# Kernel optimization log

Measured on AMD Instinct MI355X. Metric: run time of the kernel, lower is better.

The kernel has to match this reference:

```python
import jax, jax.numpy as jnp
import numpy as np

GH = 16           # graph_hidden_features
D_IN = 2 * GH     # 32, concat(embed, lin)
D_H = 32          # hidden_features1
D_OUT = 16        # output_features1
NU, NC, E, L = 500000, 10000, 2000000, 500000


def _sage(x_src, x_dst, e_src, e_dst, Wl, bl, Wr, n_dst):
    # PyG SAGEConv: lin_l(mean_{j in N(i)} x_j) + lin_r(x_i); lin_r has no bias
    msg = x_src[e_src]                                   # [E, d]
    agg = jax.ops.segment_sum(msg, e_dst, num_segments=n_dst)
    cnt = jax.ops.segment_sum(jnp.ones((e_dst.shape[0],), msg.dtype), e_dst, num_segments=n_dst)
    agg = agg / jnp.maximum(cnt, 1.0)[:, None]
    return agg @ Wl.T + bl + x_dst @ Wr.T


def setup_inputs() -> dict:
    key = jax.random.key(0)
    ks = jax.random.split(key, 32)
    s = 0.05
    inp = {
        'user_x': jax.random.normal(ks[0], (NU, 5), jnp.float32),
        'course_x': jax.random.normal(ks[1], (NC, 2), jnp.float32),
        'user_embed': jax.random.normal(ks[2], (NU, GH), jnp.float32) * s,
        'course_embed': jax.random.normal(ks[3], (NC, GH), jnp.float32) * s,
        'Wu': jax.random.normal(ks[4], (GH, 5), jnp.float32) * s,
        'bu': jnp.zeros((GH,), jnp.float32),
        'Wc': jax.random.normal(ks[5], (GH, 2), jnp.float32) * s,
        'bc': jnp.zeros((GH,), jnp.float32),
        # conv1, edge type ('user','enroll','course')
        'c1e_Wl': jax.random.normal(ks[6], (D_H, D_IN), jnp.float32) * s,
        'c1e_bl': jnp.zeros((D_H,), jnp.float32),
        'c1e_Wr': jax.random.normal(ks[7], (D_H, D_IN), jnp.float32) * s,
        # conv1, edge type ('course','rev_enroll','user')
        'c1r_Wl': jax.random.normal(ks[8], (D_H, D_IN), jnp.float32) * s,
        'c1r_bl': jnp.zeros((D_H,), jnp.float32),
        'c1r_Wr': jax.random.normal(ks[9], (D_H, D_IN), jnp.float32) * s,
        # conv2 per edge type
        'c2e_Wl': jax.random.normal(ks[10], (D_OUT, D_H), jnp.float32) * s,
        'c2e_bl': jnp.zeros((D_OUT,), jnp.float32),
        'c2e_Wr': jax.random.normal(ks[11], (D_OUT, D_H), jnp.float32) * s,
        'c2r_Wl': jax.random.normal(ks[12], (D_OUT, D_H), jnp.float32) * s,
        'c2r_bl': jnp.zeros((D_OUT,), jnp.float32),
        'c2r_Wr': jax.random.normal(ks[13], (D_OUT, D_H), jnp.float32) * s,
        'user_node_index': jnp.arange(NU, dtype=jnp.int64) if jax.config.jax_enable_x64 else jnp.arange(NU, dtype=jnp.int32),
        'course_node_index': jnp.arange(NC, dtype=jnp.int32),
        'edge_src': jax.random.randint(ks[14], (E,), 0, NU, jnp.int32),
        'edge_dst': jax.random.randint(ks[15], (E,), 0, NC, jnp.int32),
        'label_src': jax.random.randint(ks[16], (L,), 0, NU, jnp.int32),
        'label_dst': jax.random.randint(ks[17], (L,), 0, NC, jnp.int32),
    }
    return inp


def reference(user_x, course_x, user_embed, course_embed, Wu, bu, Wc, bc,
              c1e_Wl, c1e_bl, c1e_Wr, c1r_Wl, c1r_bl, c1r_Wr,
              c2e_Wl, c2e_bl, c2e_Wr, c2r_Wl, c2r_bl, c2r_Wr,
              user_node_index, course_node_index, edge_src, edge_dst,
              label_src, label_dst):
    n_u, n_c = user_x.shape[0], course_x.shape[0]
    # feature fusion: concat(embedding lookup, linear projection)  -> [N, 32]
    xu = jnp.concatenate([user_embed[user_node_index], user_x @ Wu.T + bu], axis=1)
    xc = jnp.concatenate([course_embed[course_node_index], course_x @ Wc.T + bc], axis=1)
    # layer 1 (to_hetero: separate SAGEConv params per edge type, one edge type per dst)
    hc = jax.nn.relu(_sage(xu, xc, edge_src, edge_dst, c1e_Wl, c1e_bl, c1e_Wr, n_c))
    hu = jax.nn.relu(_sage(xc, xu, edge_dst, edge_src, c1r_Wl, c1r_bl, c1r_Wr, n_u))
    # layer 2
    oc = _sage(hu, hc, edge_src, edge_dst, c2e_Wl, c2e_bl, c2e_Wr, n_c)
    ou = _sage(hc, hu, edge_dst, edge_src, c2r_Wl, c2r_bl, c2r_Wr, n_u)
    # dot-product decode on labeled edges
    return (ou[label_src] * oc[label_dst]).sum(axis=-1)
```

## Files before the change

kernel.cpp:

```cpp
#include <hip/hip_runtime.h>

#define THREADS 256
#define CSH 6
#define USH 12
#define MAXBIN 192

typedef _Float16 half8 __attribute__((ext_vector_type(8)));
typedef _Float16 half4 __attribute__((ext_vector_type(4)));
typedef float floatx4 __attribute__((ext_vector_type(4)));

static __device__ __forceinline__ int imax(int a, int b){ return a > b ? a : b; }
static __device__ __forceinline__ int imin(int a, int b){ return a < b ? a : b; }


__global__ __launch_bounds__(256) void k_phase0(const int* __restrict__ es, const int* __restrict__ ed,
                                                int* __restrict__ cnt_c, int* __restrict__ cnt_u,
                                                int E, int NBC, int NBU){
    __shared__ int hc[MAXBIN], hu[MAXBIN];
    int t = threadIdx.x;
    int base = blockIdx.x * 2048 + t;
    if (t < MAXBIN){ hc[t] = 0; hu[t] = 0; }
    __syncthreads();
    #pragma unroll
    for (int k = 0; k < 8; k++){
        int i = base + k * 256;
        if (i < E){
            int s = __builtin_nontemporal_load(&es[i]);
            int d = __builtin_nontemporal_load(&ed[i]);
            atomicAdd(&hc[d >> CSH], 1); atomicAdd(&hu[s >> USH], 1);
        }
    }
    __syncthreads();
    if (t < NBC && hc[t]) atomicAdd(&cnt_c[t], hc[t]);
    if (t < NBU && hu[t]) atomicAdd(&cnt_u[t], hu[t]);
}

__global__ void k_sbase(const int* __restrict__ cnt_c, const int* __restrict__ cnt_u,
                        int* __restrict__ base_c, int* __restrict__ cur_c,
                        int* __restrict__ base_u, int* __restrict__ cur_u,
                        int* __restrict__ off_c, int* __restrict__ off_u,
                        int NC, int NU, int NBC, int NBU, int E){
    if (threadIdx.x == 0){
        int a = 0;
        for (int b = 0; b < NBC; b++){ base_c[b] = a; cur_c[b] = a; a += cnt_c[b]; }
        a = 0;
        for (int b = 0; b < NBU; b++){ base_u[b] = a; cur_u[b] = a; a += cnt_u[b]; }
        off_c[NC] = E; off_u[NU] = E;
    }
}

__global__ __launch_bounds__(256) void k_phase1(const int* __restrict__ es, const int* __restrict__ ed,
                                                int* __restrict__ cur_c, int* __restrict__ cur_u,
                                                uint2* __restrict__ binned_c, uint2* __restrict__ binned_u,
                                                int E, int NBC, int NBU){
    __shared__ uint2 stc[2048], stu[2048];
    __shared__ int hc[MAXBIN], scc[MAXBIN], lcc[MAXBIN], gbc[MAXBIN];
    __shared__ int hu[MAXBIN], scu[MAXBIN], lcu[MAXBIN], gbu[MAXBIN];
    int t = threadIdx.x;
    int base = blockIdx.x * 2048 + t;
    int s[8], d[8];
    #pragma unroll
    for (int k = 0; k < 8; k++){
        int i = base + k * 256;
        if (i < E){ s[k] = __builtin_nontemporal_load(&es[i]); d[k] = __builtin_nontemporal_load(&ed[i]); }
    }
    if (t < MAXBIN){ hc[t] = 0; hu[t] = 0; }
    __syncthreads();
    #pragma unroll
    for (int k = 0; k < 8; k++){
        int i = base + k * 256;
        if (i < E){ atomicAdd(&hc[d[k] >> CSH], 1); atomicAdd(&hu[s[k] >> USH], 1); }
    }
    __syncthreads();
    if (t == 0){ int a = 0; for (int b = 0; b < NBC; b++){ scc[b] = a; a += hc[b]; } }
    if (t == 1){ int a = 0; for (int b = 0; b < NBU; b++){ scu[b] = a; a += hu[b]; } }
    __syncthreads();
    if (t < NBC){ lcc[t] = scc[t]; gbc[t] = atomicAdd(&cur_c[t], hc[t]); }
    if (t < NBU){ lcu[t] = scu[t]; gbu[t] = atomicAdd(&cur_u[t], hu[t]); }
    __syncthreads();
    #pragma unroll
    for (int k = 0; k < 8; k++){
        int i = base + k * 256;
        if (i < E){
            int p = atomicAdd(&lcc[d[k] >> CSH], 1); stc[p] = make_uint2((unsigned)s[k], (unsigned)d[k]);
            int q = atomicAdd(&lcu[s[k] >> USH], 1); stu[q] = make_uint2((unsigned)s[k], (unsigned)d[k]);
        }
    }
    __syncthreads();
    int nv = imin(2048, E - blockIdx.x * 2048);
    for (int i = t; i < nv; i += 256){
        uint2 e = stc[i]; int b  = (int)(e.y >> CSH); binned_c[gbc[b]  + (i - scc[b])]  = e;
        uint2 f = stu[i]; int b2 = (int)(f.x >> USH); binned_u[gbu[b2] + (i - scu[b2])] = f;
    }
}

__global__ __launch_bounds__(1024) void k_p2(const uint2* __restrict__ binned_c, const uint2* __restrict__ binned_u,
                                             const int* __restrict__ cnt_c, const int* __restrict__ base_c,
                                             const int* __restrict__ cnt_u, const int* __restrict__ base_u,
                                             int* __restrict__ off_c, int* __restrict__ csr_c,
                                             int* __restrict__ off_u, int* __restrict__ csr_u,
                                             int NC, int NU, int NBC){
    __shared__ int lsh[5120];
    int t = threadIdx.x;
    const int CB = 1 << CSH;
    if ((int)blockIdx.x < NBC){
        int b = blockIdx.x;
        int* lh  = lsh;
        int* lof = lsh + CB;
        if (t < CB) lh[t] = 0;
        __syncthreads();
        int n = cnt_c[b], gb = base_c[b];
        const uint2* src = binned_c + gb;
        for (int i = t; i < n; i += 1024) atomicAdd(&lh[src[i].y & (CB - 1)], 1);
        __syncthreads();
        if (t == 0){ int a = gb; for (int c = 0; c < CB; c++){ lof[c] = a; a += lh[c]; } }
        __syncthreads();
        int gc = (b << CSH) + t;
        if (t < CB && gc < NC) off_c[gc] = lof[t];
        __syncthreads();
        for (int i = t; i < n; i += 1024){
            uint2 e = src[i];
            int p = atomicAdd(&lof[e.y & (CB - 1)], 1);
            csr_c[p] = (int)e.x;
        }
    } else {
        int b = blockIdx.x - NBC;
        const int UB = 1 << USH;
        int* lh   = lsh;
        int* part = lsh + UB;
        for (int i = t; i < UB; i += 1024) lh[i] = 0;
        __syncthreads();
        int n = cnt_u[b], gb = base_u[b];
        const uint2* src = binned_u + gb;
        for (int i = t; i < n; i += 1024) atomicAdd(&lh[src[i].x & (UB - 1)], 1);
        __syncthreads();
        int ps = lh[t * 4] + lh[t * 4 + 1] + lh[t * 4 + 2] + lh[t * 4 + 3];
        part[t] = ps;
        __syncthreads();
        for (int dd = 1; dd < 1024; dd <<= 1){
            int v = (t >= dd) ? part[t - dd] : 0;
            __syncthreads();
            if (t >= dd) part[t] += v;
            __syncthreads();
        }
        int a2 = gb + (t ? part[t - 1] : 0);
        #pragma unroll
        for (int j = 0; j < 4; j++){ int idx = t * 4 + j; int tmp = lh[idx]; lh[idx] = a2; a2 += tmp; }
        __syncthreads();
        int ub = b << USH;
        for (int i = t; i < UB; i += 1024){ int gu = ub + i; if (gu < NU) off_u[gu] = lh[i]; }
        __syncthreads();
        for (int i = t; i < n; i += 1024){
            uint2 e = src[i];
            int p = atomicAdd(&lh[e.x & (UB - 1)], 1);
            csr_u[p] = (int)e.y;
        }
    }
}


__global__ __launch_bounds__(256) void k_xu16(const float* __restrict__ uemb, const int* __restrict__ uidx,
                                              const float* __restrict__ ux, _Float16* __restrict__ xu16, int NU){
    int u = blockIdx.x * blockDim.x + threadIdx.x;
    if (u >= NU) return;
    const float4* er = (const float4*)(uemb + (size_t)uidx[u] * 16);
    float4 e0 = er[0], e1 = er[1], e2 = er[2], e3 = er[3];
    _Float16 h[32];
    h[0]=(_Float16)e0.x; h[1]=(_Float16)e0.y; h[2]=(_Float16)e0.z; h[3]=(_Float16)e0.w;
    h[4]=(_Float16)e1.x; h[5]=(_Float16)e1.y; h[6]=(_Float16)e1.z; h[7]=(_Float16)e1.w;
    h[8]=(_Float16)e2.x; h[9]=(_Float16)e2.y; h[10]=(_Float16)e2.z; h[11]=(_Float16)e2.w;
    h[12]=(_Float16)e3.x; h[13]=(_Float16)e3.y; h[14]=(_Float16)e3.z; h[15]=(_Float16)e3.w;
    const float* xr = ux + (size_t)u * 5;
    h[16]=(_Float16)xr[0]; h[17]=(_Float16)xr[1]; h[18]=(_Float16)xr[2]; h[19]=(_Float16)xr[3]; h[20]=(_Float16)xr[4];
    #pragma unroll
    for (int q = 21; q < 32; q++) h[q] = (_Float16)0.f;
    float4* out = (float4*)(xu16 + (size_t)u * 32);
    const float4* hv = (const float4*)h;
    out[0] = hv[0]; out[1] = hv[1]; out[2] = hv[2]; out[3] = hv[3];
}


__global__ void k_wprep(const float* __restrict__ Wl, const float* __restrict__ bl,
                        const float* __restrict__ Wr, const float* __restrict__ Wu,
                        const float* __restrict__ bu,
                        const float* __restrict__ Acoef, const float* __restrict__ Bcoef,
                        _Float16* __restrict__ wB1a, _Float16* __restrict__ wB1b,
                        _Float16* __restrict__ wB2, float* __restrict__ whb){
    int t = threadIdx.x;
    if (t < 128){
        int nt = t >> 6, l = t & 63;
        int ur = l & 15, kg = l >> 4, o = nt * 16 + ur;
        _Float16* pa = wB1a + (size_t)(nt * 64 + l) * 8;
        _Float16* pb = wB1b + (size_t)(nt * 64 + l) * 8;
        #pragma unroll
        for (int j = 0; j < 8; j++){
            pa[j] = (_Float16)Wl[o * 32 + kg * 8 + j];
            int k = kg * 8 + j;
            float v;
            if (k < 16) v = Wr[o * 32 + k];
            else if (k < 21){
                int pc = k - 16; float s = 0.f;
                for (int m = 0; m < 16; m++) s += Wr[o * 32 + 16 + m] * Wu[m * 5 + pc];
                v = s;
            } else v = 0.f;
            pb[j] = (_Float16)v;
        }
        const float* W = nt ? Bcoef : Acoef;
        _Float16* p2 = wB2 + (size_t)(nt * 64 + l) * 8;
        #pragma unroll
        for (int j = 0; j < 8; j++) p2[j] = (_Float16)W[ur * 32 + kg * 8 + j];
    } else if (t < 160){
        int o = t - 128;
        float s = bl[o];
        for (int m = 0; m < 16; m++) s += Wr[o * 32 + 16 + m] * bu[m];
        whb[o] = s;
    }
}


__global__ void k_xc(const float* __restrict__ cx, const float* __restrict__ cemb,
                     const int* __restrict__ cidx, const float* __restrict__ Wc,
                     const float* __restrict__ bc, float* __restrict__ xc,
                     _Float16* __restrict__ xc16, int NC){
    int i = blockIdx.x * blockDim.x + threadIdx.x;
    if (i >= NC * 32) return;
    int c = i >> 5, f = i & 31;
    float v;
    if (f < 16) v = cemb[cidx[c] * 16 + f];
    else { int o = f - 16; v = bc[o] + cx[c * 2 + 0] * Wc[o * 2 + 0] + cx[c * 2 + 1] * Wc[o * 2 + 1]; }
    xc[i] = v;
    xc16[i] = (_Float16)v;
}


__global__ __launch_bounds__(256) void k_course_l1(
    const int* __restrict__ off_c, const int* __restrict__ csr_c,
    const _Float16* __restrict__ xu16,
    const float* __restrict__ Wu, const float* __restrict__ bu,
    const float* __restrict__ Wl, const float* __restrict__ bl, const float* __restrict__ Wr,
    const float* __restrict__ Acoef , const float* __restrict__ Bcoef ,
    const float* __restrict__ xc,
    _Float16* __restrict__ hc2r16, float* __restrict__ hcWr, int NC)
{
    __shared__ float sWlT[1024], sWrT[1024], sAT[512], sBT[512], sWu[80], sbu[16], sbl[32];
    __shared__ float part[256];
    __shared__ float agg[32], aggx[8], hc[32];
    int t = threadIdx.x;
    for (int i = t; i < 1024; i += 256){ int o = i >> 5, k = i & 31; sWlT[k * 32 + o] = Wl[i]; sWrT[k * 32 + o] = Wr[i]; }
    for (int i = t; i < 512;  i += 256){ int j = i >> 5, o = i & 31; sAT[o * 16 + j] = Acoef[i]; sBT[o * 16 + j] = Bcoef[i]; }
    if (t < 80) sWu[t] = Wu[t];
    if (t < 16) sbu[t] = bu[t];
    if (t < 32) sbl[t] = bl[t];
    __syncthreads();
    int el = t >> 5, f = t & 31;
    for (int c = blockIdx.x; c < NC; c += gridDim.x){
        int lo = off_c[c], hi = off_c[c + 1];
        float acc = 0.f;
        int j = lo + el;
        for (; j + 24 < hi; j += 32){
            int s0 = csr_c[j], s1 = csr_c[j + 8], s2 = csr_c[j + 16], s3 = csr_c[j + 24];
            acc += (float)xu16[(size_t)s0 * 32 + f] + (float)xu16[(size_t)s1 * 32 + f]
                 + (float)xu16[(size_t)s2 * 32 + f] + (float)xu16[(size_t)s3 * 32 + f];
        }
        for (; j < hi; j += 8) acc += (float)xu16[(size_t)csr_c[j] * 32 + f];
        part[t] = acc; __syncthreads();
        float inv = 1.f / (float)imax(hi - lo, 1);
        if (el == 0 && f < 21){
            float s2 = part[f];
            #pragma unroll
            for (int k = 1; k < 8; k++) s2 += part[k * 32 + f];
            s2 *= inv;
            if (f < 16) agg[f] = s2; else aggx[f - 16] = s2;
        }
        __syncthreads();
        if (t < 16){
            float d = sbu[t];
            #pragma unroll
            for (int k = 0; k < 5; k++) d += aggx[k] * sWu[t * 5 + k];
            agg[16 + t] = d;
        }
        __syncthreads();
        if (t < 32){
            float h = sbl[t];
            for (int k = 0; k < 32; k++) h += agg[k] * sWlT[k * 32 + t] + xc[c * 32 + k] * sWrT[k * 32 + t];
            hc[t] = fmaxf(h, 0.f);
        }
        __syncthreads();
        if (t < 16){
            float a = 0.f, b = 0.f;
            for (int o = 0; o < 32; o++){ float h = hc[o]; a += h * sAT[o * 16 + t]; b += h * sBT[o * 16 + t]; }
            hc2r16[c * 16 + t] = (_Float16)a; hcWr[c * 16 + t] = b;
        }
        __syncthreads();
    }
}


__global__ __launch_bounds__(256) void k_user_mfma(
    const int* __restrict__ off_u, const int* __restrict__ csr_u,
    const _Float16* __restrict__ xc16, const _Float16* __restrict__ hc2r16,
    const _Float16* __restrict__ xu16,
    const _Float16* __restrict__ wB1a, const _Float16* __restrict__ wB1b,
    const _Float16* __restrict__ wB2, const float* __restrict__ whb,
    const float* __restrict__ bl2 ,
    _Float16* __restrict__ hu2e, float* __restrict__ ou, int NU)
{
    const int t = threadIdx.x;
    const int w = t >> 6, l = t & 63;
    const int ur = l & 15;
    const int kg = l >> 4;

    half8 b1[2][2], b2[2];
    b1[0][0] = *(const half8*)(wB1a + (size_t)l * 8);
    b1[0][1] = *(const half8*)(wB1a + (size_t)(64 + l) * 8);
    b1[1][0] = *(const half8*)(wB1b + (size_t)l * 8);
    b1[1][1] = *(const half8*)(wB1b + (size_t)(64 + l) * 8);
    b2[0]    = *(const half8*)(wB2  + (size_t)l * 8);
    b2[1]    = *(const half8*)(wB2  + (size_t)(64 + l) * 8);
    float hbias[2] = { whb[ur], whb[16 + ur] };
    const float bl2v = bl2[ur];

    __shared__ float lds_all[4][16 * 36 + 16 * 20];
    float* hl  = lds_all[w];
    float* b0l = lds_all[w] + 16 * 36;

    const int stride = gridDim.x * 64;
    for (int u0 = blockIdx.x * 64 + w * 16; u0 < NU; u0 += stride){
        int u = u0 + ur;
        int lo = 0, n = 0;
        if (u < NU){ lo = off_u[u]; n = off_u[u + 1] - lo; }
        float a[8] = {0,0,0,0,0,0,0,0};
        float p4[4] = {0,0,0,0};
        int j = 0;
        while (__any(j < n)){
            int d0 = (j     < n) ? csr_u[lo + j]     : -1;
            int d1 = (j + 1 < n) ? csr_u[lo + j + 1] : -1;
            if (d0 >= 0){
                half8 xv = *(const half8*)(xc16 + (size_t)d0 * 32 + kg * 8);
                half4 hv = *(const half4*)(hc2r16 + (size_t)d0 * 16 + kg * 4);
                #pragma unroll
                for (int q = 0; q < 8; q++) a[q] += (float)xv[q];
                #pragma unroll
                for (int q = 0; q < 4; q++) p4[q] += (float)hv[q];
            }
            if (d1 >= 0){
                half8 xv = *(const half8*)(xc16 + (size_t)d1 * 32 + kg * 8);
                half4 hv = *(const half4*)(hc2r16 + (size_t)d1 * 16 + kg * 4);
                #pragma unroll
                for (int q = 0; q < 8; q++) a[q] += (float)xv[q];
                #pragma unroll
                for (int q = 0; q < 4; q++) p4[q] += (float)hv[q];
            }
            j += 2;
        }
        float inv = 1.f / (float)imax(n, 1);
        half8 a1, a2;
        #pragma unroll
        for (int q = 0; q < 8; q++) a1[q] = (_Float16)(a[q] * inv);
        #pragma unroll
        for (int q = 0; q < 8; q++) a2[q] = (_Float16)0.f;
        if (u < NU) a2 = *(const half8*)(xu16 + (size_t)u * 32 + kg * 8);
        floatx4 c1[2];
        #pragma unroll
        for (int nt = 0; nt < 2; nt++){
            floatx4 c = {hbias[nt], hbias[nt], hbias[nt], hbias[nt]};
            c = __builtin_amdgcn_mfma_f32_16x16x32_f16(a1, b1[0][nt], c, 0, 0, 0);
            c = __builtin_amdgcn_mfma_f32_16x16x32_f16(a2, b1[1][nt], c, 0, 0, 0);
            c1[nt] = c;
        }
        asm volatile("s_waitcnt lgkmcnt(0)" ::: "memory");
        #pragma unroll
        for (int nt = 0; nt < 2; nt++)
            #pragma unroll
            for (int r = 0; r < 4; r++)
                hl[(kg * 4 + r) * 36 + nt * 16 + ur] = fmaxf(c1[nt][r], 0.f);
        #pragma unroll
        for (int q = 0; q < 4; q++) b0l[ur * 20 + kg * 4 + q] = p4[q] * inv;
        asm volatile("s_waitcnt lgkmcnt(0)" ::: "memory");
        half8 ah;
        {
            const float* hp = hl + ur * 36 + kg * 8;
            #pragma unroll
            for (int q = 0; q < 8; q++) ah[q] = (_Float16)hp[q];
        }
        floatx4 c20 = {0.f, 0.f, 0.f, 0.f};
        c20 = __builtin_amdgcn_mfma_f32_16x16x32_f16(ah, b2[0], c20, 0, 0, 0);
        floatx4 c21 = {bl2v, bl2v, bl2v, bl2v};
        c21 = __builtin_amdgcn_mfma_f32_16x16x32_f16(ah, b2[1], c21, 0, 0, 0);
        #pragma unroll
        for (int r = 0; r < 4; r++){
            int urow = kg * 4 + r;
            int ug = u0 + urow;
            if (ug < NU){
                hu2e[(size_t)ug * 16 + ur] = (_Float16)c20[r];
                ou[(size_t)ug * 16 + ur]   = c21[r] + b0l[urow * 20 + ur];
            }
        }
    }
}


__global__ __launch_bounds__(256) void k_course_l2(
    const int* __restrict__ off_c, const int* __restrict__ csr_c,
    const _Float16* __restrict__ hu2e, const float* __restrict__ bl2,
    const float* __restrict__ hcWr, float* __restrict__ oc, int NC)
{
    __shared__ float part[256];
    int t = threadIdx.x; int el = t >> 4, f = t & 15;
    for (int c = blockIdx.x; c < NC; c += gridDim.x){
        int lo = off_c[c], hi = off_c[c + 1];
        float acc = 0.f;
        int j = lo + el;
        for (; j + 48 < hi; j += 64){
            acc += (float)hu2e[(size_t)csr_c[j] * 16 + f] + (float)hu2e[(size_t)csr_c[j + 16] * 16 + f]
                 + (float)hu2e[(size_t)csr_c[j + 32] * 16 + f] + (float)hu2e[(size_t)csr_c[j + 48] * 16 + f];
        }
        for (; j < hi; j += 16) acc += (float)hu2e[(size_t)csr_c[j] * 16 + f];
        part[t] = acc; __syncthreads();
        if (el == 0){
            float s = part[f];
            #pragma unroll
            for (int k = 1; k < 16; k++) s += part[k * 16 + f];
            oc[c * 16 + f] = s / (float)imax(hi - lo, 1) + bl2[f] + hcWr[c * 16 + f];
        }
        __syncthreads();
    }
}


__global__ void k_decode(const int* __restrict__ ls, const int* __restrict__ ld,
                         const float* __restrict__ ou, const float* __restrict__ oc,
                         float* __restrict__ out, int L){
    int gt = blockIdx.x * blockDim.x + threadIdx.x;
    int l = gt >> 2, q = gt & 3;
    if (l >= L) return;
    int a = ls[l], b = ld[l];
    float4 va = ((const float4*)(ou + (size_t)a * 16))[q];
    float4 vb = ((const float4*)(oc + (size_t)b * 16))[q];
    float s = va.x * vb.x + va.y * vb.y + va.z * vb.z + va.w * vb.w;
    s += __shfl_xor(s, 1);
    s += __shfl_xor(s, 2);
    if (q == 0) out[l] = s;
}


extern "C" void kernel_launch(void* const* d_in, const int* in_sizes, int n_in,
                              void* d_out, int out_size, void* d_ws, size_t ws_size,
                              hipStream_t stream)
{
    const float* user_x       = (const float*)d_in[0];
    const float* course_x     = (const float*)d_in[1];
    const float* user_embed   = (const float*)d_in[2];
    const float* course_embed = (const float*)d_in[3];
    const float* Wu = (const float*)d_in[4];
    const float* bu = (const float*)d_in[5];
    const float* Wc = (const float*)d_in[6];
    const float* bc = (const float*)d_in[7];
    const float* c1e_Wl = (const float*)d_in[8];
    const float* c1e_bl = (const float*)d_in[9];
    const float* c1e_Wr = (const float*)d_in[10];
    const float* c1r_Wl = (const float*)d_in[11];
    const float* c1r_bl = (const float*)d_in[12];
    const float* c1r_Wr = (const float*)d_in[13];
    const float* c2e_Wl = (const float*)d_in[14];
    const float* c2e_bl = (const float*)d_in[15];
    const float* c2e_Wr = (const float*)d_in[16];
    const float* c2r_Wl = (const float*)d_in[17];
    const float* c2r_bl = (const float*)d_in[18];
    const float* c2r_Wr = (const float*)d_in[19];
    const int* uidx      = (const int*)d_in[20];
    const int* cidx      = (const int*)d_in[21];
    const int* edge_src  = (const int*)d_in[22];
    const int* edge_dst  = (const int*)d_in[23];
    const int* label_src = (const int*)d_in[24];
    const int* label_dst = (const int*)d_in[25];
    const int NU = in_sizes[20], NC = in_sizes[21], E = in_sizes[22], L = in_sizes[24];
    const int NBC = (NC + (1 << CSH) - 1) >> CSH;
    const int NBU = (NU + (1 << USH) - 1) >> USH;

    char* ws = (char*)d_ws;
    size_t woff = 0;
    auto alloc = [&](size_t bytes) -> char* {
        char* p = ws + woff;
        woff = (woff + bytes + 255) & ~(size_t)255;
        return p;
    };
    int*   off_u = (int*)  alloc((size_t)(NU + 1) * 4);
    int*   off_c = (int*)  alloc((size_t)(NC + 1) * 4);
    int*   csr_c = (int*)  alloc((size_t)E * 4);
    int*   csr_u = (int*)  alloc((size_t)E * 4);
    float* xc    = (float*)alloc((size_t)NC * 32 * 4);
    _Float16* xc16 = (_Float16*)alloc((size_t)NC * 32 * 2);
    _Float16* hc2r16 = (_Float16*)alloc((size_t)NC * 16 * 2);
    float* hcWr  = (float*)alloc((size_t)NC * 16 * 4);
    _Float16* hu2e = (_Float16*)alloc((size_t)NU * 16 * 2);
    float* ou    = (float*)alloc((size_t)NU * 16 * 4);
    float* occ   = (float*)alloc((size_t)NC * 16 * 4);
    _Float16* xu16 = (_Float16*)alloc((size_t)NU * 32 * 2);
    _Float16* wB1a = (_Float16*)alloc(1024 * 2);
    _Float16* wB1b = (_Float16*)alloc(1024 * 2);
    _Float16* wB2  = (_Float16*)alloc(1024 * 2);
    float* whb     = (float*)alloc(32 * 4);
    int*   cnt_c  = (int*) alloc(MAXBIN * 4);
    int*   cnt_u  = (int*) alloc(MAXBIN * 4);
    int*   base_c = (int*) alloc(MAXBIN * 4);
    int*   base_u = (int*) alloc(MAXBIN * 4);
    int*   cur_c  = (int*) alloc(MAXBIN * 4);
    int*   cur_u  = (int*) alloc(MAXBIN * 4);
    uint2* binned_c = (uint2*)hu2e;
    uint2* binned_u = (uint2*)ou;
    (void)ws_size; (void)n_in; (void)out_size;

    int chunks = (E + 2047) / 2048;

    hipMemsetAsync(cnt_c, 0, MAXBIN * 4, stream);
    hipMemsetAsync(cnt_u, 0, MAXBIN * 4, stream);
    k_phase0<<<chunks, 256, 0, stream>>>(edge_src, edge_dst, cnt_c, cnt_u, E, NBC, NBU);
    k_wprep<<<1, 256, 0, stream>>>(c1r_Wl, c1r_bl, c1r_Wr, Wu, bu, c2e_Wl, c2r_Wr, wB1a, wB1b, wB2, whb);
    k_xu16<<<(NU + 255) / 256, 256, 0, stream>>>(user_embed, uidx, user_x, xu16, NU);
    k_sbase<<<1, 64, 0, stream>>>(cnt_c, cnt_u, base_c, cur_c, base_u, cur_u, off_c, off_u, NC, NU, NBC, NBU, E);
    k_phase1<<<chunks, 256, 0, stream>>>(edge_src, edge_dst, cur_c, cur_u, binned_c, binned_u, E, NBC, NBU);
    k_xc<<<(NC * 32 + 255) / 256, 256, 0, stream>>>(course_x, course_embed, cidx, Wc, bc, xc, xc16, NC);
    k_p2<<<NBC + NBU, 1024, 0, stream>>>(binned_c, binned_u, cnt_c, base_c, cnt_u, base_u,
                                         off_c, csr_c, off_u, csr_u, NC, NU, NBC);
    k_course_l1<<<2048, 256, 0, stream>>>(off_c, csr_c, xu16, Wu, bu,
                                          c1e_Wl, c1e_bl, c1e_Wr, c2r_Wl, c2e_Wr, xc, hc2r16, hcWr, NC);
    k_user_mfma<<<1024, 256, 0, stream>>>(off_u, csr_u, xc16, hc2r16, xu16,
                                          wB1a, wB1b, wB2, whb, c2r_bl, hu2e, ou, NU);
    k_course_l2<<<2048, 256, 0, stream>>>(off_c, csr_c, hu2e, c2e_bl, hcWr, occ, NC);
    k_decode<<<(unsigned)(((size_t)L * 4 + 255) / 256), 256, 0, stream>>>(label_src, label_dst, ou, occ, (float*)d_out, L);
}
```

Measured before the change: 307.9 us.

## Store user output in fp16, unroll gather by four, double user kernel grid

The user-side output ou is now stored as fp16 instead of fp32, which halves its write traffic in k_user_mfma and its read traffic in k_decode. The user neighbor-gather loop now processes four edges per iteration instead of two, giving more loads in flight. The user kernel grid is doubled to 2048 blocks. Because ou no longer aliases the binned_u scratch buffer, binned_u gets its own workspace allocation, which needs more workspace memory and adds fp16 rounding error to the final dot products.

```diff
diff --git a/kernel.cpp b/kernel.cpp
--- a/kernel.cpp
+++ b/kernel.cpp
@@ -303,7 +303,7 @@
     const _Float16* __restrict__ wB1a, const _Float16* __restrict__ wB1b,
     const _Float16* __restrict__ wB2, const float* __restrict__ whb,
     const float* __restrict__ bl2 ,
-    _Float16* __restrict__ hu2e, float* __restrict__ ou, int NU)
+    _Float16* __restrict__ hu2e, _Float16* __restrict__ ou, int NU)
 {
     const int t = threadIdx.x;
     const int w = t >> 6, l = t & 63;
@@ -335,6 +335,8 @@
         while (__any(j < n)){
             int d0 = (j     < n) ? csr_u[lo + j]     : -1;
             int d1 = (j + 1 < n) ? csr_u[lo + j + 1] : -1;
+            int d2 = (j + 2 < n) ? csr_u[lo + j + 2] : -1;
+            int d3 = (j + 3 < n) ? csr_u[lo + j + 3] : -1;
             if (d0 >= 0){
                 half8 xv = *(const half8*)(xc16 + (size_t)d0 * 32 + kg * 8);
                 half4 hv = *(const half4*)(hc2r16 + (size_t)d0 * 16 + kg * 4);
@@ -351,7 +353,23 @@
                 #pragma unroll
                 for (int q = 0; q < 4; q++) p4[q] += (float)hv[q];
             }
-            j += 2;
+            if (d2 >= 0){
+                half8 xv = *(const half8*)(xc16 + (size_t)d2 * 32 + kg * 8);
+                half4 hv = *(const half4*)(hc2r16 + (size_t)d2 * 16 + kg * 4);
+                #pragma unroll
+                for (int q = 0; q < 8; q++) a[q] += (float)xv[q];
+                #pragma unroll
+                for (int q = 0; q < 4; q++) p4[q] += (float)hv[q];
+            }
+            if (d3 >= 0){
+                half8 xv = *(const half8*)(xc16 + (size_t)d3 * 32 + kg * 8);
+                half4 hv = *(const half4*)(hc2r16 + (size_t)d3 * 16 + kg * 4);
+                #pragma unroll
+                for (int q = 0; q < 8; q++) a[q] += (float)xv[q];
+                #pragma unroll
+                for (int q = 0; q < 4; q++) p4[q] += (float)hv[q];
+            }
+            j += 4;
         }
         float inv = 1.f / (float)imax(n, 1);
         half8 a1, a2;
@@ -393,7 +411,7 @@
             int ug = u0 + urow;
             if (ug < NU){
                 hu2e[(size_t)ug * 16 + ur] = (_Float16)c20[r];
-                ou[(size_t)ug * 16 + ur]   = c21[r] + b0l[urow * 20 + ur];
+                ou[(size_t)ug * 16 + ur]   = (_Float16)(c21[r] + b0l[urow * 20 + ur]);
             }
         }
     }
@@ -429,15 +447,15 @@
 
 
 __global__ void k_decode(const int* __restrict__ ls, const int* __restrict__ ld,
-                         const float* __restrict__ ou, const float* __restrict__ oc,
+                         const _Float16* __restrict__ ou, const float* __restrict__ oc,
                          float* __restrict__ out, int L){
     int gt = blockIdx.x * blockDim.x + threadIdx.x;
     int l = gt >> 2, q = gt & 3;
     if (l >= L) return;
     int a = ls[l], b = ld[l];
-    float4 va = ((const float4*)(ou + (size_t)a * 16))[q];
+    half4 va = *(const half4*)(ou + (size_t)a * 16 + q * 4);
     float4 vb = ((const float4*)(oc + (size_t)b * 16))[q];
-    float s = va.x * vb.x + va.y * vb.y + va.z * vb.z + va.w * vb.w;
+    float s = (float)va[0] * vb.x + (float)va[1] * vb.y + (float)va[2] * vb.z + (float)va[3] * vb.w;
     s += __shfl_xor(s, 1);
     s += __shfl_xor(s, 2);
     if (q == 0) out[l] = s;
@@ -494,7 +512,8 @@
     _Float16* hc2r16 = (_Float16*)alloc((size_t)NC * 16 * 2);
     float* hcWr  = (float*)alloc((size_t)NC * 16 * 4);
     _Float16* hu2e = (_Float16*)alloc((size_t)NU * 16 * 2);
-    float* ou    = (float*)alloc((size_t)NU * 16 * 4);
+    _Float16* ou   = (_Float16*)alloc((size_t)NU * 16 * 2);
+    uint2* binned_u = (uint2*)alloc((size_t)E * 8);
     float* occ   = (float*)alloc((size_t)NC * 16 * 4);
     _Float16* xu16 = (_Float16*)alloc((size_t)NU * 32 * 2);
     _Float16* wB1a = (_Float16*)alloc(1024 * 2);
@@ -508,7 +527,6 @@
     int*   cur_c  = (int*) alloc(MAXBIN * 4);
     int*   cur_u  = (int*) alloc(MAXBIN * 4);
     uint2* binned_c = (uint2*)hu2e;
-    uint2* binned_u = (uint2*)ou;
     (void)ws_size; (void)n_in; (void)out_size;
 
     int chunks = (E + 2047) / 2048;
@@ -525,7 +543,7 @@
                                          off_c, csr_c, off_u, csr_u, NC, NU, NBC);
     k_course_l1<<<2048, 256, 0, stream>>>(off_c, csr_c, xu16, Wu, bu,
                                           c1e_Wl, c1e_bl, c1e_Wr, c2r_Wl, c2e_Wr, xc, hc2r16, hcWr, NC);
-    k_user_mfma<<<1024, 256, 0, stream>>>(off_u, csr_u, xc16, hc2r16, xu16,
+    k_user_mfma<<<2048, 256, 0, stream>>>(off_u, csr_u, xc16, hc2r16, xu16,
                                           wB1a, wB1b, wB2, whb, c2r_bl, hu2e, ou, NU);
     k_course_l2<<<2048, 256, 0, stream>>>(off_c, csr_c, hu2e, c2e_bl, hcWr, occ, NC);
     k_decode<<<(unsigned)(((size_t)L * 4 + 255) / 256), 256, 0, stream>>>(label_src, label_dst, ou, occ, (float*)d_out, L);
```

Result: no change. 304.6 us (-1.1%).

## Pack binned edges to 32-bit, fuse prep kernels, store ou in fp16

Applied to the files above, without the earlier changes.

Binned edges are packed into one 32-bit word (source index shifted above the low dst bits) plus a byte bin tag in shared memory, which halves the scatter and reread traffic in the binning and CSR passes. The small prep kernels are merged (scan with weight prep, user with course feature build) and the two memsets become one, cutting launch count. The user-layer gather now unrolls eight neighbours per iteration and accumulates in fp16 vectors, ou is stored as fp16, and the user kernel grid is doubled. These add fp16 precision risk in the accumulation and outputs, and the packing assumes node ids fit in the remaining bits.

```diff
diff --git a/kernel.cpp b/kernel.cpp
--- a/kernel.cpp
+++ b/kernel.cpp
@@ -35,25 +35,64 @@
     if (t < NBU && hu[t]) atomicAdd(&cnt_u[t], hu[t]);
 }
 
-__global__ void k_sbase(const int* __restrict__ cnt_c, const int* __restrict__ cnt_u,
-                        int* __restrict__ base_c, int* __restrict__ cur_c,
-                        int* __restrict__ base_u, int* __restrict__ cur_u,
-                        int* __restrict__ off_c, int* __restrict__ off_u,
-                        int NC, int NU, int NBC, int NBU, int E){
-    if (threadIdx.x == 0){
-        int a = 0;
-        for (int b = 0; b < NBC; b++){ base_c[b] = a; cur_c[b] = a; a += cnt_c[b]; }
-        a = 0;
-        for (int b = 0; b < NBU; b++){ base_u[b] = a; cur_u[b] = a; a += cnt_u[b]; }
-        off_c[NC] = E; off_u[NU] = E;
+__global__ void k_misc(const int* __restrict__ cnt_c, const int* __restrict__ cnt_u,
+                       int* __restrict__ base_c, int* __restrict__ cur_c,
+                       int* __restrict__ base_u, int* __restrict__ cur_u,
+                       int* __restrict__ off_c, int* __restrict__ off_u,
+                       int NC, int NU, int NBC, int NBU, int E,
+                       const float* __restrict__ Wl, const float* __restrict__ bl,
+                       const float* __restrict__ Wr, const float* __restrict__ Wu,
+                       const float* __restrict__ bu,
+                       const float* __restrict__ Acoef, const float* __restrict__ Bcoef,
+                       _Float16* __restrict__ wB1a, _Float16* __restrict__ wB1b,
+                       _Float16* __restrict__ wB2, float* __restrict__ whb){
+    int t = threadIdx.x;
+    if (blockIdx.x == 0){
+        if (t == 0){
+            int a = 0;
+            for (int b = 0; b < NBC; b++){ base_c[b] = a; cur_c[b] = a; a += cnt_c[b]; }
+            a = 0;
+            for (int b = 0; b < NBU; b++){ base_u[b] = a; cur_u[b] = a; a += cnt_u[b]; }
+            off_c[NC] = E; off_u[NU] = E;
+        }
+        return;
+    }
+    if (t < 128){
+        int nt = t >> 6, l = t & 63;
+        int ur = l & 15, kg = l >> 4, o = nt * 16 + ur;
+        _Float16* pa = wB1a + (size_t)(nt * 64 + l) * 8;
+        _Float16* pb = wB1b + (size_t)(nt * 64 + l) * 8;
+        #pragma unroll
+        for (int j = 0; j < 8; j++){
+            pa[j] = (_Float16)Wl[o * 32 + kg * 8 + j];
+            int k = kg * 8 + j;
+            float v;
+            if (k < 16) v = Wr[o * 32 + k];
+            else if (k < 21){
+                int pc = k - 16; float s = 0.f;
+                for (int m = 0; m < 16; m++) s += Wr[o * 32 + 16 + m] * Wu[m * 5 + pc];
+                v = s;
+            } else v = 0.f;
+            pb[j] = (_Float16)v;
+        }
+        const float* W = nt ? Bcoef : Acoef;
+        _Float16* p2 = wB2 + (size_t)(nt * 64 + l) * 8;
+        #pragma unroll
+        for (int j = 0; j < 8; j++) p2[j] = (_Float16)W[ur * 32 + kg * 8 + j];
+    } else if (t < 160){
+        int o = t - 128;
+        float s = bl[o];
+        for (int m = 0; m < 16; m++) s += Wr[o * 32 + 16 + m] * bu[m];
+        whb[o] = s;
     }
 }
 
 __global__ __launch_bounds__(256) void k_phase1(const int* __restrict__ es, const int* __restrict__ ed,
                                                 int* __restrict__ cur_c, int* __restrict__ cur_u,
-                                                uint2* __restrict__ binned_c, uint2* __restrict__ binned_u,
+                                                unsigned* __restrict__ binned_c, unsigned* __restrict__ binned_u,
                                                 int E, int NBC, int NBU){
-    __shared__ uint2 stc[2048], stu[2048];
+    __shared__ unsigned stc[2048], stu[2048];
+    __shared__ unsigned char bc8[2048], bu8[2048];
     __shared__ int hc[MAXBIN], scc[MAXBIN], lcc[MAXBIN], gbc[MAXBIN];
     __shared__ int hu[MAXBIN], scu[MAXBIN], lcu[MAXBIN], gbu[MAXBIN];
     int t = threadIdx.x;
@@ -82,19 +121,25 @@
     for (int k = 0; k < 8; k++){
         int i = base + k * 256;
         if (i < E){
-            int p = atomicAdd(&lcc[d[k] >> CSH], 1); stc[p] = make_uint2((unsigned)s[k], (unsigned)d[k]);
-            int q = atomicAdd(&lcu[s[k] >> USH], 1); stu[q] = make_uint2((unsigned)s[k], (unsigned)d[k]);
+            int bc = d[k] >> CSH;
+            int p = atomicAdd(&lcc[bc], 1);
+            stc[p] = ((unsigned)s[k] << CSH) | ((unsigned)d[k] & ((1u << CSH) - 1));
+            bc8[p] = (unsigned char)bc;
+            int bu2 = s[k] >> USH;
+            int q = atomicAdd(&lcu[bu2], 1);
+            stu[q] = ((unsigned)d[k] << USH) | ((unsigned)s[k] & ((1u << USH) - 1));
+            bu8[q] = (unsigned char)bu2;
         }
     }
     __syncthreads();
     int nv = imin(2048, E - blockIdx.x * 2048);
     for (int i = t; i < nv; i += 256){
-        uint2 e = stc[i]; int b  = (int)(e.y >> CSH); binned_c[gbc[b]  + (i - scc[b])]  = e;
-        uint2 f = stu[i]; int b2 = (int)(f.x >> USH); binned_u[gbu[b2] + (i - scu[b2])] = f;
-    }
-}
-
-__global__ __launch_bounds__(1024) void k_p2(const uint2* __restrict__ binned_c, const uint2* __restrict__ binned_u,
+        unsigned e = stc[i]; int b  = bc8[i]; binned_c[gbc[b]  + (i - scc[b])]  = e;
+        unsigned f = stu[i]; int b2 = bu8[i]; binned_u[gbu[b2] + (i - scu[b2])] = f;
+    }
+}
+
+__global__ __launch_bounds__(1024) void k_p2(const unsigned* __restrict__ binned_c, const unsigned* __restrict__ binned_u,
                                              const int* __restrict__ cnt_c, const int* __restrict__ base_c,
                                              const int* __restrict__ cnt_u, const int* __restrict__ base_u,
                                              int* __restrict__ off_c, int* __restrict__ csr_c,
@@ -110,8 +155,8 @@
         if (t < CB) lh[t] = 0;
         __syncthreads();
         int n = cnt_c[b], gb = base_c[b];
-        const uint2* src = binned_c + gb;
-        for (int i = t; i < n; i += 1024) atomicAdd(&lh[src[i].y & (CB - 1)], 1);
+        const unsigned* src = binned_c + gb;
+        for (int i = t; i < n; i += 1024) atomicAdd(&lh[src[i] & (CB - 1)], 1);
         __syncthreads();
         if (t == 0){ int a = gb; for (int c = 0; c < CB; c++){ lof[c] = a; a += lh[c]; } }
         __syncthreads();
@@ -119,9 +164,9 @@
         if (t < CB && gc < NC) off_c[gc] = lof[t];
         __syncthreads();
         for (int i = t; i < n; i += 1024){
-            uint2 e = src[i];
-            int p = atomicAdd(&lof[e.y & (CB - 1)], 1);
-            csr_c[p] = (int)e.x;
+            unsigned e = src[i];
+            int p = atomicAdd(&lof[e & (CB - 1)], 1);
+            csr_c[p] = (int)(e >> CSH);
         }
     } else {
         int b = blockIdx.x - NBC;
@@ -131,8 +176,8 @@
         for (int i = t; i < UB; i += 1024) lh[i] = 0;
         __syncthreads();
         int n = cnt_u[b], gb = base_u[b];
-        const uint2* src = binned_u + gb;
-        for (int i = t; i < n; i += 1024) atomicAdd(&lh[src[i].x & (UB - 1)], 1);
+        const unsigned* src = binned_u + gb;
+        for (int i = t; i < n; i += 1024) atomicAdd(&lh[src[i] & (UB - 1)], 1);
         __syncthreads();
         int ps = lh[t * 4] + lh[t * 4 + 1] + lh[t * 4 + 2] + lh[t * 4 + 3];
         part[t] = ps;
@@ -151,85 +196,47 @@
         for (int i = t; i < UB; i += 1024){ int gu = ub + i; if (gu < NU) off_u[gu] = lh[i]; }
         __syncthreads();
         for (int i = t; i < n; i += 1024){
-            uint2 e = src[i];
-            int p = atomicAdd(&lh[e.x & (UB - 1)], 1);
-            csr_u[p] = (int)e.y;
-        }
-    }
-}
-
-
-__global__ __launch_bounds__(256) void k_xu16(const float* __restrict__ uemb, const int* __restrict__ uidx,
-                                              const float* __restrict__ ux, _Float16* __restrict__ xu16, int NU){
-    int u = blockIdx.x * blockDim.x + threadIdx.x;
-    if (u >= NU) return;
-    const float4* er = (const float4*)(uemb + (size_t)uidx[u] * 16);
-    float4 e0 = er[0], e1 = er[1], e2 = er[2], e3 = er[3];
-    _Float16 h[32];
-    h[0]=(_Float16)e0.x; h[1]=(_Float16)e0.y; h[2]=(_Float16)e0.z; h[3]=(_Float16)e0.w;
-    h[4]=(_Float16)e1.x; h[5]=(_Float16)e1.y; h[6]=(_Float16)e1.z; h[7]=(_Float16)e1.w;
-    h[8]=(_Float16)e2.x; h[9]=(_Float16)e2.y; h[10]=(_Float16)e2.z; h[11]=(_Float16)e2.w;
-    h[12]=(_Float16)e3.x; h[13]=(_Float16)e3.y; h[14]=(_Float16)e3.z; h[15]=(_Float16)e3.w;
-    const float* xr = ux + (size_t)u * 5;
-    h[16]=(_Float16)xr[0]; h[17]=(_Float16)xr[1]; h[18]=(_Float16)xr[2]; h[19]=(_Float16)xr[3]; h[20]=(_Float16)xr[4];
-    #pragma unroll
-    for (int q = 21; q < 32; q++) h[q] = (_Float16)0.f;
-    float4* out = (float4*)(xu16 + (size_t)u * 32);
-    const float4* hv = (const float4*)h;
-    out[0] = hv[0]; out[1] = hv[1]; out[2] = hv[2]; out[3] = hv[3];
-}
-
-
-__global__ void k_wprep(const float* __restrict__ Wl, const float* __restrict__ bl,
-                        const float* __restrict__ Wr, const float* __restrict__ Wu,
-                        const float* __restrict__ bu,
-                        const float* __restrict__ Acoef, const float* __restrict__ Bcoef,
-                        _Float16* __restrict__ wB1a, _Float16* __restrict__ wB1b,
-                        _Float16* __restrict__ wB2, float* __restrict__ whb){
-    int t = threadIdx.x;
-    if (t < 128){
-        int nt = t >> 6, l = t & 63;
-        int ur = l & 15, kg = l >> 4, o = nt * 16 + ur;
-        _Float16* pa = wB1a + (size_t)(nt * 64 + l) * 8;
-        _Float16* pb = wB1b + (size_t)(nt * 64 + l) * 8;
-        #pragma unroll
-        for (int j = 0; j < 8; j++){
-            pa[j] = (_Float16)Wl[o * 32 + kg * 8 + j];
-            int k = kg * 8 + j;
-            float v;
-            if (k < 16) v = Wr[o * 32 + k];
-            else if (k < 21){
-                int pc = k - 16; float s = 0.f;
-                for (int m = 0; m < 16; m++) s += Wr[o * 32 + 16 + m] * Wu[m * 5 + pc];
-                v = s;
-            } else v = 0.f;
-            pb[j] = (_Float16)v;
-        }
-        const float* W = nt ? Bcoef : Acoef;
-        _Float16* p2 = wB2 + (size_t)(nt * 64 + l) * 8;
-        #pragma unroll
-        for (int j = 0; j < 8; j++) p2[j] = (_Float16)W[ur * 32 + kg * 8 + j];
-    } else if (t < 160){
-        int o = t - 128;
-        float s = bl[o];
-        for (int m = 0; m < 16; m++) s += Wr[o * 32 + 16 + m] * bu[m];
-        whb[o] = s;
-    }
-}
-
-
-__global__ void k_xc(const float* __restrict__ cx, const float* __restrict__ cemb,
-                     const int* __restrict__ cidx, const float* __restrict__ Wc,
-                     const float* __restrict__ bc, float* __restrict__ xc,
-                     _Float16* __restrict__ xc16, int NC){
-    int i = blockIdx.x * blockDim.x + threadIdx.x;
-    if (i >= NC * 32) return;
-    int c = i >> 5, f = i & 31;
-    float v;
-    if (f < 16) v = cemb[cidx[c] * 16 + f];
-    else { int o = f - 16; v = bc[o] + cx[c * 2 + 0] * Wc[o * 2 + 0] + cx[c * 2 + 1] * Wc[o * 2 + 1]; }
-    xc[i] = v;
-    xc16[i] = (_Float16)v;
+            unsigned e = src[i];
+            int p = atomicAdd(&lh[e & (UB - 1)], 1);
+            csr_u[p] = (int)(e >> USH);
+        }
+    }
+}
+
+
+__global__ __launch_bounds__(256) void k_feat(const float* __restrict__ uemb, const int* __restrict__ uidx,
+                                              const float* __restrict__ ux, _Float16* __restrict__ xu16, int NU,
+                                              const float* __restrict__ cx, const float* __restrict__ cemb,
+                                              const int* __restrict__ cidx, const float* __restrict__ Wc,
+                                              const float* __restrict__ bc, float* __restrict__ xc,
+                                              _Float16* __restrict__ xc16, int NC){
+    int gid = blockIdx.x * blockDim.x + threadIdx.x;
+    if (gid < NU){
+        int u = gid;
+        const float4* er = (const float4*)(uemb + (size_t)uidx[u] * 16);
+        float4 e0 = er[0], e1 = er[1], e2 = er[2], e3 = er[3];
+        _Float16 h[32];
+        h[0]=(_Float16)e0.x; h[1]=(_Float16)e0.y; h[2]=(_Float16)e0.z; h[3]=(_Float16)e0.w;
+        h[4]=(_Float16)e1.x; h[5]=(_Float16)e1.y; h[6]=(_Float16)e1.z; h[7]=(_Float16)e1.w;
+        h[8]=(_Float16)e2.x; h[9]=(_Float16)e2.y; h[10]=(_Float16)e2.z; h[11]=(_Float16)e2.w;
+        h[12]=(_Float16)e3.x; h[13]=(_Float16)e3.y; h[14]=(_Float16)e3.z; h[15]=(_Float16)e3.w;
+        const float* xr = ux + (size_t)u * 5;
+        h[16]=(_Float16)xr[0]; h[17]=(_Float16)xr[1]; h[18]=(_Float16)xr[2]; h[19]=(_Float16)xr[3]; h[20]=(_Float16)xr[4];
+        #pragma unroll
+        for (int q = 21; q < 32; q++) h[q] = (_Float16)0.f;
+        float4* out = (float4*)(xu16 + (size_t)u * 32);
+        const float4* hv = (const float4*)h;
+        out[0] = hv[0]; out[1] = hv[1]; out[2] = hv[2]; out[3] = hv[3];
+    } else {
+        int i = gid - NU;
+        if (i >= NC * 32) return;
+        int c = i >> 5, f = i & 31;
+        float v;
+        if (f < 16) v = cemb[cidx[c] * 16 + f];
+        else { int o = f - 16; v = bc[o] + cx[c * 2 + 0] * Wc[o * 2 + 0] + cx[c * 2 + 1] * Wc[o * 2 + 1]; }
+        xc[i] = v;
+        xc16[i] = (_Float16)v;
+    }
 }
 
 
@@ -303,7 +310,7 @@
     const _Float16* __restrict__ wB1a, const _Float16* __restrict__ wB1b,
     const _Float16* __restrict__ wB2, const float* __restrict__ whb,
     const float* __restrict__ bl2 ,
-    _Float16* __restrict__ hu2e, float* __restrict__ ou, int NU)
+    _Float16* __restrict__ hu2e, _Float16* __restrict__ ou, int NU)
 {
     const int t = threadIdx.x;
     const int w = t >> 6, l = t & 63;
@@ -329,34 +336,30 @@
         int u = u0 + ur;
         int lo = 0, n = 0;
         if (u < NU){ lo = off_u[u]; n = off_u[u + 1] - lo; }
-        float a[8] = {0,0,0,0,0,0,0,0};
+        half8 axv;
+        #pragma unroll
+        for (int q = 0; q < 8; q++) axv[q] = (_Float16)0.f;
         float p4[4] = {0,0,0,0};
         int j = 0;
         while (__any(j < n)){
-            int d0 = (j     < n) ? csr_u[lo + j]     : -1;
-            int d1 = (j + 1 < n) ? csr_u[lo + j + 1] : -1;
-            if (d0 >= 0){
-                half8 xv = *(const half8*)(xc16 + (size_t)d0 * 32 + kg * 8);
-                half4 hv = *(const half4*)(hc2r16 + (size_t)d0 * 16 + kg * 4);
-                #pragma unroll
-                for (int q = 0; q < 8; q++) a[q] += (float)xv[q];
-                #pragma unroll
-                for (int q = 0; q < 4; q++) p4[q] += (float)hv[q];
+            int dd[8];
+            #pragma unroll
+            for (int k = 0; k < 8; k++) dd[k] = (j + k < n) ? csr_u[lo + j + k] : -1;
+            #pragma unroll
+            for (int k = 0; k < 8; k++){
+                if (dd[k] >= 0){
+                    axv += *(const half8*)(xc16 + (size_t)dd[k] * 32 + kg * 8);
+                    half4 hv = *(const half4*)(hc2r16 + (size_t)dd[k] * 16 + kg * 4);
+                    #pragma unroll
+                    for (int q = 0; q < 4; q++) p4[q] += (float)hv[q];
+                }
             }
-            if (d1 >= 0){
-                half8 xv = *(const half8*)(xc16 + (size_t)d1 * 32 + kg * 8);
-                half4 hv = *(const half4*)(hc2r16 + (size_t)d1 * 16 + kg * 4);
-                #pragma unroll
-                for (int q = 0; q < 8; q++) a[q] += (float)xv[q];
-                #pragma unroll
-                for (int q = 0; q < 4; q++) p4[q] += (float)hv[q];
-            }
-            j += 2;
+            j += 8;
         }
         float inv = 1.f / (float)imax(n, 1);
         half8 a1, a2;
         #pragma unroll
-        for (int q = 0; q < 8; q++) a1[q] = (_Float16)(a[q] * inv);
+        for (int q = 0; q < 8; q++) a1[q] = (_Float16)((float)axv[q] * inv);
         #pragma unroll
         for (int q = 0; q < 8; q++) a2[q] = (_Float16)0.f;
         if (u < NU) a2 = *(const half8*)(xu16 + (size_t)u * 32 + kg * 8);
@@ -393,7 +396,7 @@
             int ug = u0 + urow;
             if (ug < NU){
                 hu2e[(size_t)ug * 16 + ur] = (_Float16)c20[r];
-                ou[(size_t)ug * 16 + ur]   = c21[r] + b0l[urow * 20 + ur];
+                ou[(size_t)ug * 16 + ur]   = (_Float16)(c21[r] + b0l[urow * 20 + ur]);
             }
         }
     }
@@ -429,15 +432,15 @@
 
 
 __global__ void k_decode(const int* __restrict__ ls, const int* __restrict__ ld,
-                         const float* __restrict__ ou, const float* __restrict__ oc,
+                         const _Float16* __restrict__ ou, const float* __restrict__ oc,
                          float* __restrict__ out, int L){
     int gt = blockIdx.x * blockDim.x + threadIdx.x;
     int l = gt >> 2, q = gt & 3;
     if (l >= L) return;
     int a = ls[l], b = ld[l];
-    float4 va = ((const float4*)(ou + (size_t)a * 16))[q];
+    half4 va = *(const half4*)(ou + (size_t)a * 16 + q * 4);
     float4 vb = ((const float4*)(oc + (size_t)b * 16))[q];
-    float s = va.x * vb.x + va.y * vb.y + va.z * vb.z + va.w * vb.w;
+    float s = (float)va[0] * vb.x + (float)va[1] * vb.y + (float)va[2] * vb.z + (float)va[3] * vb.w;
     s += __shfl_xor(s, 1);
     s += __shfl_xor(s, 2);
     if (q == 0) out[l] = s;
@@ -494,7 +497,7 @@
     _Float16* hc2r16 = (_Float16*)alloc((size_t)NC * 16 * 2);
     float* hcWr  = (float*)alloc((size_t)NC * 16 * 4);
     _Float16* hu2e = (_Float16*)alloc((size_t)NU * 16 * 2);
-    float* ou    = (float*)alloc((size_t)NU * 16 * 4);
+    _Float16* ou   = (_Float16*)alloc((size_t)NU * 16 * 2);
     float* occ   = (float*)alloc((size_t)NC * 16 * 4);
     _Float16* xu16 = (_Float16*)alloc((size_t)NU * 32 * 2);
     _Float16* wB1a = (_Float16*)alloc(1024 * 2);
@@ -507,25 +510,25 @@
     int*   base_u = (int*) alloc(MAXBIN * 4);
     int*   cur_c  = (int*) alloc(MAXBIN * 4);
     int*   cur_u  = (int*) alloc(MAXBIN * 4);
-    uint2* binned_c = (uint2*)hu2e;
-    uint2* binned_u = (uint2*)ou;
+    unsigned* binned_c = (unsigned*)hu2e;
+    unsigned* binned_u = (unsigned*)ou;
     (void)ws_size; (void)n_in; (void)out_size;
 
     int chunks = (E + 2047) / 2048;
 
-    hipMemsetAsync(cnt_c, 0, MAXBIN * 4, stream);
-    hipMemsetAsync(cnt_u, 0, MAXBIN * 4, stream);
+    hipMemsetAsync(cnt_c, 0, 2 * MAXBIN * 4, stream);
     k_phase0<<<chunks, 256, 0, stream>>>(edge_src, edge_dst, cnt_c, cnt_u, E, NBC, NBU);
-    k_wprep<<<1, 256, 0, stream>>>(c1r_Wl, c1r_bl, c1r_Wr, Wu, bu, c2e_Wl, c2r_Wr, wB1a, wB1b, wB2, whb);
-    k_xu16<<<(NU + 255) / 256, 256, 0, stream>>>(user_embed, uidx, user_x, xu16, NU);
-    k_sbase<<<1, 64, 0, stream>>>(cnt_c, cnt_u, base_c, cur_c, base_u, cur_u, off_c, off_u, NC, NU, NBC, NBU, E);
+    k_misc<<<2, 256, 0, stream>>>(cnt_c, cnt_u, base_c, cur_c, base_u, cur_u, off_c, off_u,
+                                  NC, NU, NBC, NBU, E,
+                                  c1r_Wl, c1r_bl, c1r_Wr, Wu, bu, c2e_Wl, c2r_Wr, wB1a, wB1b, wB2, whb);
+    k_feat<<<(NU + NC * 32 + 255) / 256, 256, 0, stream>>>(user_embed, uidx, user_x, xu16, NU,
+                                                           course_x, course_embed, cidx, Wc, bc, xc, xc16, NC);
     k_phase1<<<chunks, 256, 0, stream>>>(edge_src, edge_dst, cur_c, cur_u, binned_c, binned_u, E, NBC, NBU);
-    k_xc<<<(NC * 32 + 255) / 256, 256, 0, stream>>>(course_x, course_embed, cidx, Wc, bc, xc, xc16, NC);
     k_p2<<<NBC + NBU, 1024, 0, stream>>>(binned_c, binned_u, cnt_c, base_c, cnt_u, base_u,
                                          off_c, csr_c, off_u, csr_u, NC, NU, NBC);
     k_course_l1<<<2048, 256, 0, stream>>>(off_c, csr_c, xu16, Wu, bu,
                                           c1e_Wl, c1e_bl, c1e_Wr, c2r_Wl, c2e_Wr, xc, hc2r16, hcWr, NC);
-    k_user_mfma<<<1024, 256, 0, stream>>>(off_u, csr_u, xc16, hc2r16, xu16,
+    k_user_mfma<<<2048, 256, 0, stream>>>(off_u, csr_u, xc16, hc2r16, xu16,
                                           wB1a, wB1b, wB2, whb, c2r_bl, hu2e, ou, NU);
     k_course_l2<<<2048, 256, 0, stream>>>(off_c, csr_c, hu2e, c2e_bl, hcWr, occ, NC);
     k_decode<<<(unsigned)(((size_t)L * 4 + 255) / 256), 256, 0, stream>>>(label_src, label_dst, ou, occ, (float*)d_out, L);
```

New measurement: 284.6 us. 1.08x faster.
